# Optimization experiments

Hardware: AMD Instinct MI355X
Metric: run time of the kernel (lower is better)

Reference implementation:

```python
import jax, jax.numpy as jnp
import numpy as np

H = 1024          # hidden_size
NH = 16           # num_attention_heads
HD = H // NH      # attention_head_size (= rotary_dim)
I = 4096          # intermediate_size
E = 8             # num_experts
TOPK = 2          # top_k_experts
EPS = 1e-12       # layer_norm_eps
B, S = 2, 2048


def setup_inputs() -> dict:
    key = jax.random.key(0)
    ks = jax.random.split(key, 12)
    sc = 0.02
    return {
        "hidden_states": jax.random.normal(ks[0], (B, S, H), dtype=jnp.float32),
        "Wq": jax.random.normal(ks[1], (H, H), dtype=jnp.float32) * sc,
        "Wk": jax.random.normal(ks[2], (H, H), dtype=jnp.float32) * sc,
        "Wv": jax.random.normal(ks[3], (H, H), dtype=jnp.float32) * sc,
        "Wd": jax.random.normal(ks[4], (H, H), dtype=jnp.float32) * sc,
        "bd": jnp.zeros((H,), dtype=jnp.float32),
        "ln1_g": jnp.ones((H,), dtype=jnp.float32),
        "ln1_b": jnp.zeros((H,), dtype=jnp.float32),
        "Wg": jax.random.normal(ks[5], (H, E), dtype=jnp.float32) * sc,
        "W1": jax.random.normal(ks[6], (E, H, I), dtype=jnp.float32) * sc,
        "W2": jax.random.normal(ks[7], (E, I, H), dtype=jnp.float32) * sc,
        "ln2_g": jnp.ones((H,), dtype=jnp.float32),
        "ln2_b": jnp.zeros((H,), dtype=jnp.float32),
    }


def _layernorm(x, g, b):
    mu = jnp.mean(x, axis=-1, keepdims=True)
    var = jnp.mean(jnp.square(x - mu), axis=-1, keepdims=True)
    return (x - mu) * jax.lax.rsqrt(var + EPS) * g + b


def _rotate_half(x):
    x1, x2 = x[..., : HD // 2], x[..., HD // 2 :]
    return jnp.concatenate((-x2, x1), axis=-1)


def _rope_cos_sin(seq_len, dtype):
    inv_freq = 1.0 / (10000.0 ** (jnp.arange(0, HD, 2, dtype=jnp.float32) / HD))
    t = jnp.arange(seq_len, dtype=jnp.float32)
    freqs = jnp.einsum("i,j->ij", t, inv_freq)          # [S, HD/2]
    emb = jnp.concatenate((freqs, freqs), axis=-1)        # [S, HD]
    return jnp.cos(emb).astype(dtype)[None, None], jnp.sin(emb).astype(dtype)[None, None]


def reference(hidden_states, Wq, Wk, Wv, Wd, bd, ln1_g, ln1_b, Wg, W1, W2, ln2_g, ln2_b):
    b, s, h = hidden_states.shape
    x = hidden_states

    # ---- multi-head attention with RoPE ----
    def heads(z):  # [B,S,H] -> [B,NH,S,HD]
        return z.reshape(b, s, NH, HD).transpose(0, 2, 1, 3)

    q = heads(x @ Wq)
    k = heads(x @ Wk)
    v = heads(x @ Wv)
    cos, sin = _rope_cos_sin(s, q.dtype)
    q = q * cos + _rotate_half(q) * sin
    k = k * cos + _rotate_half(k) * sin

    scores = jnp.einsum("bnqd,bnkd->bnqk", q, k) / jnp.sqrt(jnp.float32(HD)).astype(q.dtype)
    probs = jax.nn.softmax(scores, axis=-1)
    ctx = jnp.einsum("bnqk,bnkd->bnqd", probs, v)
    ctx = ctx.transpose(0, 2, 1, 3).reshape(b, s, h)

    attn_out = ctx @ Wd + bd
    hs = _layernorm(attn_out + x, ln1_g, ln1_b)  # residual + LN

    # ---- MoE ----
    T = b * s
    xt = hs.reshape(T, h)
    router_logits = xt @ Wg                                   # [T, E]
    probs_r = jax.nn.softmax(router_logits.astype(jnp.float32), axis=-1)
    rw, sel = jax.lax.top_k(probs_r, TOPK)                    # [T, K]
    rw = rw / jnp.sum(rw, axis=-1, keepdims=True)

    # aux load-balancing loss
    f_i = jnp.sum(jax.nn.one_hot(sel, E, dtype=jnp.float32), axis=(0, 1)) / T
    P_i = jnp.mean(probs_r, axis=0)
    aux_loss = E * jnp.sum(f_i * P_i)

    # per-token combine weights [T, E] (0 for unrouted experts)
    combine = jnp.zeros((T, E), dtype=jnp.float32)
    combine = combine.at[jnp.arange(T)[:, None], sel].add(rw)
    combine = combine.astype(xt.dtype)

    moe_out = jnp.zeros_like(xt)
    for e in range(E):  # small fixed expert loop
        ye = jax.nn.gelu(xt @ W1[e], approximate=False) @ W2[e]
        moe_out = moe_out + combine[:, e : e + 1] * ye
    moe_out = moe_out.reshape(b, s, h)

    out = _layernorm(hs + moe_out, ln2_g, ln2_b)
    return out, aux_loss
```

## Files before the change

### kernel.cpp

```cpp
#include <hip/hip_runtime.h>
#include <hip/hip_bf16.h>
#include <math.h>

#define H_ 1024
#define NH_ 16
#define HD_ 64
#define I_ 4096
#define E_ 8
#define B_ 2
#define S_ 2048
#define T_ 4096

#define MAXSLOTS 9216
#define MAXTILES 72

typedef __attribute__((ext_vector_type(8))) short short8v;
typedef __attribute__((ext_vector_type(4))) float f32x4;

#define GLOAD16(g, l) __builtin_amdgcn_global_load_lds((const __attribute__((address_space(1))) void*)(g), (__attribute__((address_space(3))) void*)(l), 16, 0, 0)

static __device__ inline unsigned short f2bf(float x) {
    __hip_bfloat16 h = __float2bfloat16(x);
    unsigned short u;
    __builtin_memcpy(&u, &h, 2);
    return u;
}
static __device__ inline float bf2f(unsigned short u) {
    __hip_bfloat16 h;
    __builtin_memcpy(&h, &u, 2);
    return __bfloat162float(h);
}

static __device__ inline float gelu_fast(float x) {
    float z  = x * 0.70710678118654752f;
    float az = fabsf(z);
    float t  = __builtin_amdgcn_rcpf(fmaf(0.3275911f, az, 1.f));
    float p  = fmaf(1.061405429f, t, -1.453152027f);
    p = fmaf(p, t, 1.421413741f);
    p = fmaf(p, t, -0.284496736f);
    p = fmaf(p, t, 0.254829592f);
    p = p * t;
    float e = __expf(-az*az);
    float er = 1.f - p*e;
    er = (z < 0.f) ? -er : er;
    return 0.5f * x * (1.f + er);
}

__global__ void zero_kernel(float* __restrict__ p, int n) {
    int i = blockIdx.x * blockDim.x + threadIdx.x;
    if (i < n) p[i] = 0.f;
}

__global__ __launch_bounds__(256) void split_bf16(
    const float* __restrict__ in, __hip_bfloat16* __restrict__ hi,
    __hip_bfloat16* __restrict__ lo, int n4)
{
    int i = blockIdx.x * blockDim.x + threadIdx.x;
    if (i >= n4) return;
    float4 v = ((const float4*)in)[i];
    unsigned short h0 = f2bf(v.x), h1 = f2bf(v.y), h2 = f2bf(v.z), h3 = f2bf(v.w);
    unsigned short l0 = f2bf(v.x - bf2f(h0)), l1 = f2bf(v.y - bf2f(h1));
    unsigned short l2 = f2bf(v.z - bf2f(h2)), l3 = f2bf(v.w - bf2f(h3));
    uint2 ph = make_uint2((unsigned)h0 | ((unsigned)h1 << 16), (unsigned)h2 | ((unsigned)h3 << 16));
    uint2 pl = make_uint2((unsigned)l0 | ((unsigned)l1 << 16), (unsigned)l2 | ((unsigned)l3 << 16));
    *(uint2*)((char*)hi + (size_t)i*8) = ph;
    *(uint2*)((char*)lo + (size_t)i*8) = pl;
}

__global__ __launch_bounds__(256) void transpose_split_w4(
    const float* __restrict__ Wq, const float* __restrict__ Wk,
    const float* __restrict__ Wv, const float* __restrict__ Wd,
    __hip_bfloat16* __restrict__ wqkv_h, __hip_bfloat16* __restrict__ wqkv_l,
    __hip_bfloat16* __restrict__ wd_h, __hip_bfloat16* __restrict__ wd_l)
{
    __shared__ float t[64][65];
    const int z = blockIdx.z;
    const float* in = (z==0) ? Wq : (z==1) ? Wk : (z==2) ? Wv : Wd;
    __hip_bfloat16* oh = (z<3) ? (wqkv_h + (size_t)z*1024*1024) : wd_h;
    __hip_bfloat16* ol = (z<3) ? (wqkv_l + (size_t)z*1024*1024) : wd_l;
    int k0 = blockIdx.y*64, n0 = blockIdx.x*64;
    int tid = threadIdx.x;
    #pragma unroll
    for (int it=0; it<4; ++it) {
        int lin = it*256 + tid;
        int r = lin >> 4, c4 = (lin & 15) << 2;
        float4 v = *(const float4*)&in[(size_t)(k0+r)*1024 + n0 + c4];
        t[r][c4] = v.x; t[r][c4+1] = v.y; t[r][c4+2] = v.z; t[r][c4+3] = v.w;
    }
    __syncthreads();
    #pragma unroll
    for (int it=0; it<4; ++it) {
        int lin = it*256 + tid;
        int r = lin >> 4, c4 = (lin & 15) << 2;
        float v0 = t[c4][r], v1 = t[c4+1][r], v2 = t[c4+2][r], v3 = t[c4+3][r];
        ushort4 hh, ll;
        hh.x = f2bf(v0); hh.y = f2bf(v1); hh.z = f2bf(v2); hh.w = f2bf(v3);
        ll.x = f2bf(v0 - bf2f(hh.x)); ll.y = f2bf(v1 - bf2f(hh.y));
        ll.z = f2bf(v2 - bf2f(hh.z)); ll.w = f2bf(v3 - bf2f(hh.w));
        size_t o = (size_t)(n0+r)*1024 + k0 + c4;
        *(ushort4*)&oh[o] = hh;
        *(ushort4*)&ol[o] = ll;
    }
}

__global__ __launch_bounds__(256) void transpose_bf16(
    const float* __restrict__ in, __hip_bfloat16* __restrict__ outp, int K, int N)
{
    __shared__ float t[64][65];
    size_t eoff = (size_t)blockIdx.z * (size_t)K * (size_t)N;
    int k0 = blockIdx.y*64, n0 = blockIdx.x*64;
    int tid = threadIdx.x;
    #pragma unroll
    for (int it=0; it<4; ++it) {
        int lin = it*256 + tid;
        int r = lin >> 4, c4 = (lin & 15) << 2;
        float4 v = *(const float4*)&in[eoff + (size_t)(k0+r)*N + n0 + c4];
        t[r][c4] = v.x; t[r][c4+1] = v.y; t[r][c4+2] = v.z; t[r][c4+3] = v.w;
    }
    __syncthreads();
    #pragma unroll
    for (int it=0; it<4; ++it) {
        int lin = it*256 + tid;
        int r = lin >> 4, c4 = (lin & 15) << 2;
        ushort4 o;
        o.x = f2bf(t[c4][r]);   o.y = f2bf(t[c4+1][r]);
        o.z = f2bf(t[c4+2][r]); o.w = f2bf(t[c4+3][r]);
        *(ushort4*)&outp[eoff + (size_t)(n0+r)*K + k0 + c4] = o;
    }
}

template<bool BIAS>
__global__ __launch_bounds__(256, 2) void gemm_bf16x3(
    const __hip_bfloat16* __restrict__ Ah, const __hip_bfloat16* __restrict__ Al,
    const __hip_bfloat16* __restrict__ Bh, const __hip_bfloat16* __restrict__ Bl,
    float* __restrict__ C, const float* __restrict__ bias, int N, int K, int nbx)
{
    const int tid = threadIdx.x;
    const int w = tid >> 6, lane = tid & 63;
    const int wg = blockIdx.x;
    const int xcd = wg & 7, ix = wg >> 3;
    const int byc = (int)(gridDim.x >> 3) / nbx;
    const int by = xcd*byc + ix / nbx;
    const int bx = ix % nbx;

    __shared__ __align__(16) char smem[65536];
    const int AH = 0, AL = 16384, BH = 32768, BL = 49152;

    const int laneg = lane >> 3;
    const int k2sw = ((lane & 7) ^ laneg) << 4;
    const int l15 = lane & 15, l4 = lane >> 4;
    const int wr = w >> 1, wc = w & 1;

    f32x4 acc[4][4];
    #pragma unroll
    for (int m=0;m<4;m++)
        #pragma unroll
        for (int n=0;n<4;n++) acc[m][n] = (f32x4){0.f,0.f,0.f,0.f};

    for (int k0 = 0; k0 < K; k0 += 64) {
        __syncthreads();
        #pragma unroll
        for (int qq=0;qq<4;qq++) {
            int arow = by*128 + (w*4+qq)*8 + laneg;
            int brow = bx*128 + (w*4+qq)*8 + laneg;
            size_t aoff = ((size_t)arow*K + k0)*2 + k2sw;
            size_t boff = ((size_t)brow*K + k0)*2 + k2sw;
            GLOAD16((const char*)Ah + aoff, smem + AH + (w*4+qq)*1024);
            GLOAD16((const char*)Al + aoff, smem + AL + (w*4+qq)*1024);
            GLOAD16((const char*)Bh + boff, smem + BH + (w*4+qq)*1024);
            GLOAD16((const char*)Bl + boff, smem + BL + (w*4+qq)*1024);
        }
        __syncthreads();

        short8v ahf[4][2], alf[4][2], bhf[4][2], blf[4][2];
        #pragma unroll
        for (int m=0;m<4;m++) {
            int row = wr*64 + m*16 + l15;
            int rb = row << 7, rsw = (row & 7) << 4;
            #pragma unroll
            for (int s=0;s<2;s++) {
                int off = rb + ((s*64 + (l4<<4)) ^ rsw);
                ahf[m][s] = *(const short8v*)(smem + AH + off);
                alf[m][s] = *(const short8v*)(smem + AL + off);
            }
        }
        #pragma unroll
        for (int n=0;n<4;n++) {
            int row = wc*64 + n*16 + l15;
            int rb = row << 7, rsw = (row & 7) << 4;
            #pragma unroll
            for (int s=0;s<2;s++) {
                int off = rb + ((s*64 + (l4<<4)) ^ rsw);
                bhf[n][s] = *(const short8v*)(smem + BH + off);
                blf[n][s] = *(const short8v*)(smem + BL + off);
            }
        }
        #pragma unroll
        for (int m=0;m<4;m++)
            #pragma unroll
            for (int n=0;n<4;n++)
                #pragma unroll
                for (int s=0;s<2;s++) {
                    acc[m][n] = __builtin_amdgcn_mfma_f32_16x16x32_bf16(ahf[m][s], bhf[n][s], acc[m][n], 0, 0, 0);
                    acc[m][n] = __builtin_amdgcn_mfma_f32_16x16x32_bf16(ahf[m][s], blf[n][s], acc[m][n], 0, 0, 0);
                    acc[m][n] = __builtin_amdgcn_mfma_f32_16x16x32_bf16(alf[m][s], bhf[n][s], acc[m][n], 0, 0, 0);
                }
    }

    #pragma unroll
    for (int m=0;m<4;m++)
        #pragma unroll
        for (int j=0;j<4;j++) {
            int orow = by*128 + wr*64 + m*16 + l4*4 + j;
            #pragma unroll
            for (int n=0;n<4;n++) {
                int ocol = bx*128 + wc*64 + n*16 + l15;
                float v = acc[m][n][j];
                if (BIAS) v += bias[ocol];
                C[(size_t)orow*N + ocol] = v;
            }
        }
}

template<int MODE, bool PE>
__global__ __launch_bounds__(256) void moe_mfma(
    const __hip_bfloat16* __restrict__ A,
    const __hip_bfloat16* __restrict__ Bt,
    __hip_bfloat16* __restrict__ y1,
    float* __restrict__ moe_out,
    const int* __restrict__ slot_token,
    const float* __restrict__ slot_w,
    const int* __restrict__ tile_expert,
    const int* __restrict__ cnt_ptr,
    const int* __restrict__ base_ptr,
    int N, int K, int nbx)
{
    const int tid = threadIdx.x;
    const int w = tid >> 6, lane = tid & 63;

    int bx, slot0, y1row0;
    const __hip_bfloat16* Bp;
    if (PE) {
        bx = blockIdx.x;
        int tloc = blockIdx.y;
        if ((tloc << 7) >= *cnt_ptr) return;
        slot0 = *base_ptr + (tloc << 7);
        y1row0 = tloc << 7;
        Bp = Bt;
    } else {
        const int wg = blockIdx.x;
        const int xcd = wg & 7, ix = wg >> 3;
        const int byc = (int)(gridDim.x >> 3) / nbx;
        int gt = xcd*byc + ix % byc;
        bx = ix / byc;
        if (gt >= *cnt_ptr) return;
        int e = tile_expert[gt];
        Bp = Bt + (size_t)e * (size_t)K * (size_t)N;
        slot0 = gt << 7;
        y1row0 = gt << 7;
    }

    __shared__ __align__(16) char smem[32768];

    const int laneg = lane >> 3;
    const int k2sw = ((lane & 7) ^ laneg) << 4;

    int tokq[4];
    if (MODE == 2) {
        #pragma unroll
        for (int qq=0;qq<4;qq++) {
            int t0 = slot_token[slot0 + (w*4+qq)*8 + laneg];
            tokq[qq] = t0 < 0 ? 0 : t0;
        }
    }

    f32x4 acc[4][4];
    #pragma unroll
    for (int m=0;m<4;m++)
        #pragma unroll
        for (int n=0;n<4;n++) acc[m][n] = (f32x4){0.f,0.f,0.f,0.f};

    const int l15 = lane & 15;
    const int l4  = lane >> 4;
    const int wr = w >> 1, wc = w & 1;

    for (int k0 = 0; k0 < K; k0 += 64) {
        __syncthreads();
        #pragma unroll
        for (int qq=0;qq<4;qq++) {
            const char* ga;
            if (MODE == 2) {
                ga = (const char*)A + (((size_t)tokq[qq])*K + k0)*2 + k2sw;
            } else {
                int row = y1row0 + (w*4+qq)*8 + laneg;
                ga = (const char*)A + ((size_t)row*K + k0)*2 + k2sw;
            }
            GLOAD16(ga, smem + (w*4+qq)*1024);
        }
        #pragma unroll
        for (int qq=0;qq<4;qq++) {
            int row = bx*128 + (w*4+qq)*8 + laneg;
            const char* gb = (const char*)Bp + ((size_t)row*K + k0)*2 + k2sw;
            GLOAD16(gb, smem + 16384 + (w*4+qq)*1024);
        }
        __syncthreads();

        short8v a_frag[4][2], b_frag[4][2];
        #pragma unroll
        for (int m=0;m<4;m++) {
            int row = wr*64 + m*16 + l15;
            int rb = row << 7;
            #pragma unroll
            for (int s=0;s<2;s++) {
                int off = rb + ((s*64 + (l4<<4)) ^ ((row&7)<<4));
                a_frag[m][s] = *(const short8v*)(smem + off);
            }
        }
        #pragma unroll
        for (int n=0;n<4;n++) {
            int row = wc*64 + n*16 + l15;
            int rb = row << 7;
            #pragma unroll
            for (int s=0;s<2;s++) {
                int off = rb + ((s*64 + (l4<<4)) ^ ((row&7)<<4));
                b_frag[n][s] = *(const short8v*)(smem + 16384 + off);
            }
        }
        #pragma unroll
        for (int m=0;m<4;m++)
            #pragma unroll
            for (int n=0;n<4;n++) {
                acc[m][n] = __builtin_amdgcn_mfma_f32_16x16x32_bf16(a_frag[m][0], b_frag[n][0], acc[m][n], 0, 0, 0);
                acc[m][n] = __builtin_amdgcn_mfma_f32_16x16x32_bf16(a_frag[m][1], b_frag[n][1], acc[m][n], 0, 0, 0);
            }
    }

    if (MODE == 3) {
        #pragma unroll
        for (int m=0;m<4;m++) {
            #pragma unroll
            for (int j=0;j<4;j++) {
                int orow = wr*64 + m*16 + l4*4 + j;
                int slot = slot0 + orow;
                int tok = slot_token[slot];
                if (tok < 0) continue;
                float sw = slot_w[slot];
                #pragma unroll
                for (int n=0;n<4;n++) {
                    int ocol = bx*128 + wc*64 + n*16 + l15;
                    atomicAdd(&moe_out[(size_t)tok*H_ + ocol], sw * acc[m][n][j]);
                }
            }
        }
    } else {
        __syncthreads();
        #pragma unroll
        for (int m=0;m<4;m++)
            #pragma unroll
            for (int j=0;j<4;j++) {
                int orow = wr*64 + m*16 + l4*4 + j;
                #pragma unroll
                for (int n=0;n<4;n++) {
                    int ocol = wc*64 + n*16 + l15;
                    unsigned short g = f2bf(gelu_fast(acc[m][n][j]));
                    *(unsigned short*)(smem + orow*256 + ocol*2) = g;
                }
            }
        __syncthreads();
        #pragma unroll
        for (int s=0;s<8;s++) {
            int row = w*32 + s*4 + l4;
            short8v v = *(const short8v*)(smem + row*256 + l15*16);
            *(short8v*)((char*)y1 + ((size_t)(y1row0 + row)*N + bx*128 + l15*8)*2) = v;
        }
    }
}

__global__ void rope_split_kernel(
    const float* __restrict__ qkv,
    __hip_bfloat16* __restrict__ qh, __hip_bfloat16* __restrict__ ql,
    __hip_bfloat16* __restrict__ kh, __hip_bfloat16* __restrict__ kl)
{
    int idx = blockIdx.x * blockDim.x + threadIdx.x;
    int i = idx & 31;
    int n = (idx >> 5) & (NH_-1);
    int t = idx >> 9;
    int b = t >> 11;
    int pos = t & (S_ - 1);
    float inv = exp2f((float)i * (-13.287712379549449f / 32.f));
    float ang = (float)pos * inv;
    float c = cosf(ang), s = sinf(ang);
    size_t base = (size_t)t*3072 + (size_t)n*64;
    size_t obase = ((size_t)(b*NH_ + n)*S_ + pos)*64;

    float q1 = qkv[base+i], q2 = qkv[base+i+32];
    float qo1 = (q1*c - q2*s)*0.125f;
    float qo2 = (q2*c + q1*s)*0.125f;
    unsigned short h1 = f2bf(qo1), h2 = f2bf(qo2);
    qh[obase+i]    = *(__hip_bfloat16*)&h1;
    qh[obase+i+32] = *(__hip_bfloat16*)&h2;
    unsigned short lo1 = f2bf(qo1 - bf2f(h1)), lo2 = f2bf(qo2 - bf2f(h2));
    ql[obase+i]    = *(__hip_bfloat16*)&lo1;
    ql[obase+i+32] = *(__hip_bfloat16*)&lo2;

    float k1 = qkv[base+1024+i], k2 = qkv[base+1024+i+32];
    float ko1 = k1*c - k2*s;
    float ko2 = k2*c + k1*s;
    unsigned short kh1 = f2bf(ko1), kh2 = f2bf(ko2);
    kh[obase+i]    = *(__hip_bfloat16*)&kh1;
    kh[obase+i+32] = *(__hip_bfloat16*)&kh2;
    unsigned short kl1 = f2bf(ko1 - bf2f(kh1)), kl2 = f2bf(ko2 - bf2f(kh2));
    kl[obase+i]    = *(__hip_bfloat16*)&kl1;
    kl[obase+i+32] = *(__hip_bfloat16*)&kl2;
}

__global__ __launch_bounds__(256) void vsplit_t_kernel(
    const float* __restrict__ qkv,
    __hip_bfloat16* __restrict__ vth, __hip_bfloat16* __restrict__ vtl)
{
    __shared__ float t[64][65];
    const int s0 = blockIdx.x*64;
    const int hn = blockIdx.y;
    const int b  = blockIdx.z;
    const int tid = threadIdx.x;
    #pragma unroll
    for (int it=0; it<4; ++it) {
        int lin = it*256 + tid;
        int r = lin >> 4, c4 = (lin & 15) << 2;
        float4 vv = *(const float4*)&qkv[(size_t)(b*S_ + s0 + r)*3072 + 2048 + hn*64 + c4];
        t[r][c4] = vv.x; t[r][c4+1] = vv.y; t[r][c4+2] = vv.z; t[r][c4+3] = vv.w;
    }
    __syncthreads();
    size_t obase = (size_t)(b*NH_ + hn)*64*S_;
    #pragma unroll
    for (int it=0; it<4; ++it) {
        int lin = it*256 + tid;
        int d = lin >> 4, c4 = (lin & 15) << 2;
        float v0 = t[c4][d], v1 = t[c4+1][d], v2 = t[c4+2][d], v3 = t[c4+3][d];
        ushort4 hh, ll;
        hh.x = f2bf(v0); hh.y = f2bf(v1); hh.z = f2bf(v2); hh.w = f2bf(v3);
        ll.x = f2bf(v0 - bf2f(hh.x)); ll.y = f2bf(v1 - bf2f(hh.y));
        ll.z = f2bf(v2 - bf2f(hh.z)); ll.w = f2bf(v3 - bf2f(hh.w));
        size_t o = obase + (size_t)d*S_ + s0 + c4;
        *(ushort4*)&vth[o] = hh;
        *(ushort4*)&vtl[o] = ll;
    }
}

__global__ __launch_bounds__(256) void attn_mfma(
    const __hip_bfloat16* __restrict__ qh, const __hip_bfloat16* __restrict__ ql,
    const __hip_bfloat16* __restrict__ kh, const __hip_bfloat16* __restrict__ kl,
    const __hip_bfloat16* __restrict__ vth, const __hip_bfloat16* __restrict__ vtl,
    __hip_bfloat16* __restrict__ ctx_hi, __hip_bfloat16* __restrict__ ctx_lo)
{
    const int wg = blockIdx.x;
    const int xcd = wg & 7;
    const int ix = wg >> 3;
    const int head = xcd*4 + (ix >> 5);
    const int qt = ix & 31;
    const int b = head >> 4, hn = head & 15;

    const int tid = threadIdx.x;
    const int w = tid >> 6, lane = tid & 63;
    const int l15 = lane & 15, l4 = lane >> 4;
    const int laneg = lane >> 3;
    const int k2sw = ((lane & 7) ^ laneg) << 4;

    __shared__ __align__(16) char smem[32768];
    const int KHo = 0, KLo = 8192, VHo = 16384, VLo = 24576;
    const int PHo = 0, PLo = 8192;

    const size_t kbase = (size_t)head*S_*64;
    const size_t vbase = (size_t)head*64*S_;

    #pragma unroll
    for (int qq=0;qq<2;qq++) {
        int c = w*2 + qq;
        int row = qt*64 + c*8 + laneg;
        size_t off = (kbase + (size_t)row*64)*2 + k2sw;
        GLOAD16((const char*)qh + off, smem + KHo + c*1024);
        GLOAD16((const char*)ql + off, smem + KLo + c*1024);
    }
    __syncthreads();
    short8v qhf[2], qlf[2];
    {
        int row = w*16 + l15;
        int rsw = (row & 7) << 4;
        #pragma unroll
        for (int s=0;s<2;s++) {
            int off = row*128 + ((s*64 + l4*16) ^ rsw);
            qhf[s] = *(const short8v*)(smem + KHo + off);
            qlf[s] = *(const short8v*)(smem + KLo + off);
        }
    }

    f32x4 acc[4];
    #pragma unroll
    for (int db=0;db<4;db++) acc[db] = (f32x4){0.f,0.f,0.f,0.f};
    float lrun[4] = {0.f, 0.f, 0.f, 0.f};

    for (int kt=0; kt<S_/64; ++kt) {
        __syncthreads();
        #pragma unroll
        for (int qq=0;qq<2;qq++) {
            int c = w*2 + qq;
            int r8 = c*8 + laneg;
            size_t koff = (kbase + (size_t)(kt*64 + r8)*64)*2 + k2sw;
            GLOAD16((const char*)kh + koff, smem + KHo + c*1024);
            GLOAD16((const char*)kl + koff, smem + KLo + c*1024);
            size_t voff = (vbase + (size_t)r8*S_ + kt*64)*2 + k2sw;
            GLOAD16((const char*)vth + voff, smem + VHo + c*1024);
            GLOAD16((const char*)vtl + voff, smem + VLo + c*1024);
        }
        __syncthreads();

        f32x4 s_acc[4];
        #pragma unroll
        for (int cb=0;cb<4;cb++) {
            s_acc[cb] = (f32x4){0.f,0.f,0.f,0.f};
            int row = cb*16 + l15;
            int rsw = (row & 7) << 4;
            #pragma unroll
            for (int s=0;s<2;s++) {
                int off = row*128 + ((s*64 + l4*16) ^ rsw);
                short8v khf = *(const short8v*)(smem + KHo + off);
                short8v klf = *(const short8v*)(smem + KLo + off);
                s_acc[cb] = __builtin_amdgcn_mfma_f32_16x16x32_bf16(qhf[s], khf, s_acc[cb], 0, 0, 0);
                s_acc[cb] = __builtin_amdgcn_mfma_f32_16x16x32_bf16(qhf[s], klf, s_acc[cb], 0, 0, 0);
                s_acc[cb] = __builtin_amdgcn_mfma_f32_16x16x32_bf16(qlf[s], khf, s_acc[cb], 0, 0, 0);
            }
        }
        __syncthreads();

        #pragma unroll
        for (int cb=0;cb<4;cb++)
            #pragma unroll
            for (int j=0;j<4;j++) {
                float p = __expf(s_acc[cb][j]);
                lrun[j] += p;
                int prow = w*16 + l4*4 + j;
                unsigned short hh = f2bf(p);
                unsigned short ll = f2bf(p - bf2f(hh));
                int off = prow*128 + (((cb*16 + l15)*2) ^ ((prow&7)<<4));
                *(unsigned short*)(smem + PHo + off) = hh;
                *(unsigned short*)(smem + PLo + off) = ll;
            }
        asm volatile("s_waitcnt lgkmcnt(0)" ::: "memory");
        __builtin_amdgcn_sched_barrier(0);

        short8v pah[2], pal[2];
        {
            int row = w*16 + l15;
            int rsw = (row & 7) << 4;
            #pragma unroll
            for (int s=0;s<2;s++) {
                int off = row*128 + ((s*64 + l4*16) ^ rsw);
                pah[s] = *(const short8v*)(smem + PHo + off);
                pal[s] = *(const short8v*)(smem + PLo + off);
            }
        }
        #pragma unroll
        for (int db=0;db<4;db++) {
            int row = db*16 + l15;
            int rsw = (row & 7) << 4;
            #pragma unroll
            for (int s=0;s<2;s++) {
                int off = row*128 + ((s*64 + l4*16) ^ rsw);
                short8v vhf = *(const short8v*)(smem + VHo + off);
                short8v vlf = *(const short8v*)(smem + VLo + off);
                acc[db] = __builtin_amdgcn_mfma_f32_16x16x32_bf16(pah[s], vhf, acc[db], 0, 0, 0);
                acc[db] = __builtin_amdgcn_mfma_f32_16x16x32_bf16(pah[s], vlf, acc[db], 0, 0, 0);
                acc[db] = __builtin_amdgcn_mfma_f32_16x16x32_bf16(pal[s], vhf, acc[db], 0, 0, 0);
            }
        }
    }

    #pragma unroll
    for (int j=0;j<4;j++) {
        float s = lrun[j];
        #pragma unroll
        for (int m=8;m;m>>=1) s += __shfl_xor(s, m);
        lrun[j] = s;
    }

    #pragma unroll
    for (int db=0;db<4;db++)
        #pragma unroll
        for (int j=0;j<4;j++) {
            int qrow = qt*64 + w*16 + l4*4 + j;
            float o = acc[db][j] / lrun[j];
            unsigned short hh = f2bf(o);
            unsigned short ll = f2bf(o - bf2f(hh));
            size_t oidx = (size_t)(b*S_ + qrow)*H_ + hn*64 + db*16 + l15;
            ctx_hi[oidx] = *(__hip_bfloat16*)&hh;
            ctx_lo[oidx] = *(__hip_bfloat16*)&ll;
        }
}

__global__ __launch_bounds__(256) void ln_kernel(
    const float* __restrict__ a, const float* __restrict__ res,
    const float* __restrict__ g, const float* __restrict__ beta,
    float* __restrict__ out, __hip_bfloat16* __restrict__ outb)
{
    int row = blockIdx.x, tid = threadIdx.x;
    const float4 va = ((const float4*)(a + (size_t)row*H_))[tid];
    const float4 vr = ((const float4*)(res + (size_t)row*H_))[tid];
    float x0=va.x+vr.x, x1=va.y+vr.y, x2=va.z+vr.z, x3=va.w+vr.w;
    float s  = x0+x1+x2+x3;
    float ss = x0*x0 + x1*x1 + x2*x2 + x3*x3;
    #pragma unroll
    for (int off=32; off; off>>=1) { s += __shfl_xor(s, off); ss += __shfl_xor(ss, off); }
    __shared__ float red[8];
    if ((tid&63)==0) { red[tid>>6]=s; red[4+(tid>>6)]=ss; }
    __syncthreads();
    if (tid==0) { red[0]=red[0]+red[1]+red[2]+red[3]; red[4]=red[4]+red[5]+red[6]+red[7]; }
    __syncthreads();
    float mu  = red[0] * (1.f/H_);
    float var = red[4] * (1.f/H_) - mu*mu;
    float rs = rsqrtf(fmaxf(var, 0.f) + 1e-12f);
    const float4 vg = ((const float4*)g)[tid];
    const float4 vb = ((const float4*)beta)[tid];
    float4 vo;
    vo.x = (x0-mu)*rs*vg.x + vb.x;
    vo.y = (x1-mu)*rs*vg.y + vb.y;
    vo.z = (x2-mu)*rs*vg.z + vb.z;
    vo.w = (x3-mu)*rs*vg.w + vb.w;
    ((float4*)(out + (size_t)row*H_))[tid] = vo;
    if (outb) {
        unsigned int p0 = (unsigned)f2bf(vo.x) | ((unsigned)f2bf(vo.y) << 16);
        unsigned int p1 = (unsigned)f2bf(vo.z) | ((unsigned)f2bf(vo.w) << 16);
        ((uint2*)(outb + (size_t)row*H_))[tid] = make_uint2(p0, p1);
    }
}

__global__ __launch_bounds__(256) void router_kernel(
    const float* __restrict__ hs, const float* __restrict__ Wg,
    int* __restrict__ tok_e, float* __restrict__ tok_w,
    int* __restrict__ counts, float* __restrict__ P_sum)
{
    const int w = threadIdx.x >> 6, lane = threadIdx.x & 63;
    float psum[E_];
    int cnt[E_];
    #pragma unroll
    for (int e=0;e<E_;e++){ psum[e]=0.f; cnt[e]=0; }

    for (int it=0; it<16; ++it) {
        int t = blockIdx.x*64 + it*4 + w;
        const float* row = hs + (size_t)t * H_;
        float acc[E_];
        #pragma unroll
        for (int e=0;e<E_;e++) acc[e]=0.f;
        for (int i16=0; i16<16; ++i16) {
            int i = i16*64 + lane;
            float xv = row[i];
            const float* wg = Wg + (size_t)i*E_;
            #pragma unroll
            for (int e=0;e<E_;e++) acc[e] = fmaf(xv, wg[e], acc[e]);
        }
        #pragma unroll
        for (int e=0;e<E_;e++) {
            float vv = acc[e];
            #pragma unroll
            for (int off=32; off; off>>=1) vv += __shfl_xor(vv, off);
            acc[e] = vv;
        }
        float mx = acc[0];
        #pragma unroll
        for (int e=1;e<E_;e++) mx = fmaxf(mx, acc[e]);
        float p[E_], se=0.f;
        #pragma unroll
        for (int e=0;e<E_;e++){ p[e] = __expf(acc[e]-mx); se += p[e]; }
        float isv = 1.f/se;
        #pragma unroll
        for (int e=0;e<E_;e++){ p[e]*=isv; psum[e] += p[e]; }
        int e1=0;
        #pragma unroll
        for (int e=1;e<E_;e++) if (p[e] > p[e1]) e1=e;
        int e2 = (e1==0)?1:0;
        #pragma unroll
        for (int e=0;e<E_;e++) if (e!=e1 && p[e] > p[e2]) e2=e;
        #pragma unroll
        for (int e=0;e<E_;e++) cnt[e] += (e==e1?1:0) + (e==e2?1:0);
        if (lane==0) {
            float w1=p[e1], w2=p[e2], si=1.f/(w1+w2);
            tok_e[t*2]=e1; tok_e[t*2+1]=e2;
            tok_w[t*2]=w1*si; tok_w[t*2+1]=w2*si;
        }
    }
    if (lane==0) {
        #pragma unroll
        for (int e=0;e<E_;e++) {
            atomicAdd(&P_sum[e], psum[e]);
            atomicAdd(&counts[e], cnt[e]);
        }
    }
}

__global__ void router_finalize(
    const int* __restrict__ counts, const float* __restrict__ P_sum,
    int* __restrict__ base, int* __restrict__ cursor,
    int* __restrict__ cnt_pad, int* __restrict__ ntiles,
    int* __restrict__ slot_token, int* __restrict__ tile_expert,
    float* __restrict__ aux_out)
{
    __shared__ int sbase[E_+1];
    if (threadIdx.x == 0) {
        int bacc = 0;
        float aux = 0.f;
        for (int e=0;e<E_;e++) {
            sbase[e] = bacc; base[e] = bacc;
            int cp = (counts[e] + 127) & ~127;
            cnt_pad[e] = cp;
            bacc += cp;
            cursor[e] = 0;
            aux += ((float)counts[e]/(float)T_) * (P_sum[e]/(float)T_);
        }
        sbase[E_] = bacc;
        *ntiles = bacc >> 7;
        *aux_out = (float)E_ * aux;
    }
    __syncthreads();
    for (int sIdx = (int)threadIdx.x; sIdx < MAXSLOTS; sIdx += (int)blockDim.x)
        slot_token[sIdx] = -1;
    for (int tt = (int)threadIdx.x; tt < MAXTILES; tt += (int)blockDim.x) {
        int s = tt*128;
        int e = E_-1;
        for (int qe=0; qe<E_; ++qe) if (s < sbase[qe+1]) { e = qe; break; }
        tile_expert[tt] = e;
    }
}

__global__ void scatter_slots(
    const int* __restrict__ tok_e, const float* __restrict__ tok_w,
    const int* __restrict__ base, int* __restrict__ cursor,
    int* __restrict__ slot_token, float* __restrict__ slot_w)
{
    int t = blockIdx.x*blockDim.x + threadIdx.x;
    if (t >= T_) return;
    #pragma unroll
    for (int j=0;j<2;j++) {
        int e = tok_e[t*2+j];
        int pos = atomicAdd(&cursor[e], 1);
        int s = base[e] + pos;
        slot_token[s] = t;
        slot_w[s] = tok_w[t*2+j];
    }
}

extern "C" void kernel_launch(void* const* d_in, const int* in_sizes, int n_in,
                              void* d_out, int out_size, void* d_ws, size_t ws_size,
                              hipStream_t stream)
{
    const float* x    = (const float*)d_in[0];
    const float* Wq   = (const float*)d_in[1];
    const float* Wk   = (const float*)d_in[2];
    const float* Wv   = (const float*)d_in[3];
    const float* Wd   = (const float*)d_in[4];
    const float* bd   = (const float*)d_in[5];
    const float* ln1g = (const float*)d_in[6];
    const float* ln1b = (const float*)d_in[7];
    const float* Wg   = (const float*)d_in[8];
    const float* W1   = (const float*)d_in[9];
    const float* W2   = (const float*)d_in[10];
    const float* ln2g = (const float*)d_in[11];
    const float* ln2b = (const float*)d_in[12];
    float* out = (float*)d_out;

    float* f0 = (float*)d_ws;
    const size_t M1 = 1u << 20;
    float* qkv      = f0;
    float* attn_out = f0 + 12*M1;
    float* hs       = f0;
    float* moe_out  = f0 + 4*M1;
    __hip_bfloat16* hs_b = (__hip_bfloat16*)(f0 + 16*M1);

    float* misc = f0 + 18*M1;
    int*   misc_i = (int*)misc;
    int*   tok_e   = misc_i;
    float* tok_w   = misc + 8192;
    int*   slot_tok= misc_i + 16384;
    float* slot_w  = misc + 25600;
    int*   counts  = misc_i + 34816;
    float* P_sum   = misc + 34824;
    int*   cursor  = misc_i + 34832;
    int*   basep   = misc_i + 34840;
    int*   cnt_pad = misc_i + 34848;
    int*   ntiles  = misc_i + 34856;
    int*   tile_ex = misc_i + 34857;

    float* off_p = f0 + 18*M1 + 65536;
    __hip_bfloat16* xa_hi = (__hip_bfloat16*)(off_p);
    __hip_bfloat16* xa_lo = (__hip_bfloat16*)(off_p + 2*M1);
    __hip_bfloat16* at_qh = (__hip_bfloat16*)(off_p + 4*M1);
    __hip_bfloat16* at_ql = (__hip_bfloat16*)(off_p + 6*M1);
    __hip_bfloat16* at_kh = (__hip_bfloat16*)(off_p + 8*M1);
    __hip_bfloat16* at_kl = (__hip_bfloat16*)(off_p + 10*M1);
    __hip_bfloat16* at_vh = (__hip_bfloat16*)(off_p + 12*M1);
    __hip_bfloat16* at_vl = (__hip_bfloat16*)(off_p + 14*M1);
    __hip_bfloat16* wqkv_h = (__hip_bfloat16*)(off_p + 16*M1);
    __hip_bfloat16* wqkv_l = (__hip_bfloat16*)(off_p + 16*M1 + 3*(M1/2));
    __hip_bfloat16* wd_h = (__hip_bfloat16*)(off_p + 19*M1);
    __hip_bfloat16* wd_l = (__hip_bfloat16*)(off_p + 19*M1 + M1/2);

    float* wreg = off_p + 4*M1;
    const bool FULL = ws_size >= (size_t)300*1024*1024;

    dim3 blk(256);

    split_bf16<<<(T_*H_/4)/256, blk, 0, stream>>>(x, xa_hi, xa_lo, T_*H_/4);
    transpose_split_w4<<<dim3(16,16,4), blk, 0, stream>>>(Wq, Wk, Wv, Wd, wqkv_h, wqkv_l, wd_h, wd_l);

    gemm_bf16x3<false><<<dim3(768), blk, 0, stream>>>(xa_hi, xa_lo, wqkv_h, wqkv_l, qkv, nullptr, 3072, H_, 24);

    rope_split_kernel<<<(T_*NH_*32)/256, blk, 0, stream>>>(qkv, at_qh, at_ql, at_kh, at_kl);
    vsplit_t_kernel<<<dim3(S_/64, NH_, B_), blk, 0, stream>>>(qkv, at_vh, at_vl);

    attn_mfma<<<dim3(B_*NH_*(S_/64)), blk, 0, stream>>>(at_qh, at_ql, at_kh, at_kl, at_vh, at_vl, xa_hi, xa_lo);

    gemm_bf16x3<true><<<dim3(256), blk, 0, stream>>>(xa_hi, xa_lo, wd_h, wd_l, attn_out, bd, H_, H_, 8);

    zero_kernel<<<(T_*H_)/256, blk, 0, stream>>>(moe_out, T_*H_);
    zero_kernel<<<1, blk, 0, stream>>>(misc + 34816, 16);

    ln_kernel<<<T_, blk, 0, stream>>>(attn_out, x, ln1g, ln1b, hs, hs_b);

    router_kernel<<<T_/64, blk, 0, stream>>>(hs, Wg, tok_e, tok_w, counts, P_sum);
    router_finalize<<<1, blk, 0, stream>>>(counts, P_sum, basep, cursor, cnt_pad, ntiles,
                                           slot_tok, tile_ex, out + (size_t)T_*H_);
    scatter_slots<<<T_/256, blk, 0, stream>>>(tok_e, tok_w, basep, cursor, slot_tok, slot_w);

    if (FULL) {
        __hip_bfloat16* W1t = (__hip_bfloat16*)wreg;
        __hip_bfloat16* W2t = (__hip_bfloat16*)(wreg + 16*M1);
        __hip_bfloat16* y1  = (__hip_bfloat16*)(wreg + 32*M1);
        transpose_bf16<<<dim3(I_/64, H_/64, E_), blk, 0, stream>>>(W1, W1t, H_, I_);
        transpose_bf16<<<dim3(H_/64, I_/64, E_), blk, 0, stream>>>(W2, W2t, I_, H_);
        moe_mfma<2,false><<<dim3(MAXTILES*32), blk, 0, stream>>>(
            hs_b, W1t, y1, nullptr, slot_tok, slot_w, tile_ex, ntiles, nullptr, I_, H_, 32);
        moe_mfma<3,false><<<dim3(MAXTILES*8), blk, 0, stream>>>(
            y1, W2t, nullptr, moe_out, slot_tok, slot_w, tile_ex, ntiles, nullptr, H_, I_, 8);
    } else {
        __hip_bfloat16* w1t = (__hip_bfloat16*)wreg;
        __hip_bfloat16* w2t = (__hip_bfloat16*)(wreg + 2*M1);
        __hip_bfloat16* y1  = (__hip_bfloat16*)(wreg + 4*M1);
        for (int e=0; e<E_; ++e) {
            transpose_bf16<<<dim3(I_/64, H_/64, 1), blk, 0, stream>>>(W1 + (size_t)e*H_*I_, w1t, H_, I_);
            moe_mfma<2,true><<<dim3(I_/128, 32), blk, 0, stream>>>(
                hs_b, w1t, y1, nullptr, slot_tok, slot_w, nullptr, cnt_pad+e, basep+e, I_, H_, 0);
            transpose_bf16<<<dim3(H_/64, I_/64, 1), blk, 0, stream>>>(W2 + (size_t)e*I_*H_, w2t, I_, H_);
            moe_mfma<3,true><<<dim3(H_/128, 32), blk, 0, stream>>>(
                y1, w2t, nullptr, moe_out, slot_tok, slot_w, nullptr, cnt_pad+e, basep+e, H_, I_, 0);
        }
    }

    ln_kernel<<<T_, blk, 0, stream>>>(moe_out, hs, ln2g, ln2b, out, nullptr);
}
```

Measured before the change: 762.6 us.

## Fuse prep kernels and overlap MoE weight transposes with the QKV GEMM

Merges the input split and the QKV/Wd weight transpose-split into one launch, merges RoPE with the V transpose-split, and merges the two zeroing kernels. In the full-workspace path, the W1/W2 expert transposes move into the same grid as the QKV GEMM as extra blocks, so the memory-bound transposes can fill the GPU alongside the compute-bound GEMM. Workspace buffers are relaid so y1 and the transposed weights do not overlap buffers still in use. The fused GEMM kernel uses launch_bounds of 2, which may change register allocation compared with the standalone GEMM.

```diff
diff --git a/kernel.cpp b/kernel.cpp
--- a/kernel.cpp
+++ b/kernel.cpp
@@ -46,40 +46,41 @@
     return 0.5f * x * (1.f + er);
 }
 
-__global__ void zero_kernel(float* __restrict__ p, int n) {
+__global__ void zero_all(float* __restrict__ p, int n, float* __restrict__ misc16) {
     int i = blockIdx.x * blockDim.x + threadIdx.x;
     if (i < n) p[i] = 0.f;
-}
-
-__global__ __launch_bounds__(256) void split_bf16(
-    const float* __restrict__ in, __hip_bfloat16* __restrict__ hi,
-    __hip_bfloat16* __restrict__ lo, int n4)
-{
-    int i = blockIdx.x * blockDim.x + threadIdx.x;
-    if (i >= n4) return;
-    float4 v = ((const float4*)in)[i];
-    unsigned short h0 = f2bf(v.x), h1 = f2bf(v.y), h2 = f2bf(v.z), h3 = f2bf(v.w);
-    unsigned short l0 = f2bf(v.x - bf2f(h0)), l1 = f2bf(v.y - bf2f(h1));
-    unsigned short l2 = f2bf(v.z - bf2f(h2)), l3 = f2bf(v.w - bf2f(h3));
-    uint2 ph = make_uint2((unsigned)h0 | ((unsigned)h1 << 16), (unsigned)h2 | ((unsigned)h3 << 16));
-    uint2 pl = make_uint2((unsigned)l0 | ((unsigned)l1 << 16), (unsigned)l2 | ((unsigned)l3 << 16));
-    *(uint2*)((char*)hi + (size_t)i*8) = ph;
-    *(uint2*)((char*)lo + (size_t)i*8) = pl;
-}
-
-__global__ __launch_bounds__(256) void transpose_split_w4(
+    if (blockIdx.x == 0 && threadIdx.x < 16) misc16[threadIdx.x] = 0.f;
+}
+
+__global__ __launch_bounds__(256) void prep_inputs(
+    const float* __restrict__ x,
     const float* __restrict__ Wq, const float* __restrict__ Wk,
     const float* __restrict__ Wv, const float* __restrict__ Wd,
+    __hip_bfloat16* __restrict__ xa_hi, __hip_bfloat16* __restrict__ xa_lo,
     __hip_bfloat16* __restrict__ wqkv_h, __hip_bfloat16* __restrict__ wqkv_l,
     __hip_bfloat16* __restrict__ wd_h, __hip_bfloat16* __restrict__ wd_l)
 {
     __shared__ float t[64][65];
-    const int z = blockIdx.z;
+    const int bid = blockIdx.x;
+    const int tid = threadIdx.x;
+    if (bid < 4096) {
+        int i = bid * 256 + tid;
+        float4 v = ((const float4*)x)[i];
+        unsigned short h0 = f2bf(v.x), h1 = f2bf(v.y), h2 = f2bf(v.z), h3 = f2bf(v.w);
+        unsigned short l0 = f2bf(v.x - bf2f(h0)), l1 = f2bf(v.y - bf2f(h1));
+        unsigned short l2 = f2bf(v.z - bf2f(h2)), l3 = f2bf(v.w - bf2f(h3));
+        uint2 ph = make_uint2((unsigned)h0 | ((unsigned)h1 << 16), (unsigned)h2 | ((unsigned)h3 << 16));
+        uint2 pl = make_uint2((unsigned)l0 | ((unsigned)l1 << 16), (unsigned)l2 | ((unsigned)l3 << 16));
+        *(uint2*)((char*)xa_hi + (size_t)i*8) = ph;
+        *(uint2*)((char*)xa_lo + (size_t)i*8) = pl;
+        return;
+    }
+    int tt = bid - 4096;
+    int bx = tt & 15, by = (tt >> 4) & 15, z = tt >> 8;
     const float* in = (z==0) ? Wq : (z==1) ? Wk : (z==2) ? Wv : Wd;
     __hip_bfloat16* oh = (z<3) ? (wqkv_h + (size_t)z*1024*1024) : wd_h;
     __hip_bfloat16* ol = (z<3) ? (wqkv_l + (size_t)z*1024*1024) : wd_l;
-    int k0 = blockIdx.y*64, n0 = blockIdx.x*64;
-    int tid = threadIdx.x;
+    int k0 = by*64, n0 = bx*64;
     #pragma unroll
     for (int it=0; it<4; ++it) {
         int lin = it*256 + tid;
@@ -220,6 +221,132 @@
                 C[(size_t)orow*N + ocol] = v;
             }
         }
+}
+
+__global__ __launch_bounds__(256, 2) void fused_qkv_w12(
+    const __hip_bfloat16* __restrict__ Ah, const __hip_bfloat16* __restrict__ Al,
+    const __hip_bfloat16* __restrict__ Bh, const __hip_bfloat16* __restrict__ Bl,
+    float* __restrict__ C,
+    const float* __restrict__ W1, const float* __restrict__ W2,
+    __hip_bfloat16* __restrict__ W1t, __hip_bfloat16* __restrict__ W2t)
+{
+    __shared__ __align__(16) char smem[65536];
+    const int tid = threadIdx.x;
+    const int bid = blockIdx.x;
+
+    if (bid < 768) {
+        const int N = 3072, K = 1024;
+        const int w = tid >> 6, lane = tid & 63;
+        const int xcd = bid & 7, ix = bid >> 3;
+        const int by = xcd*4 + ix / 24;
+        const int bx = ix % 24;
+        const int AH = 0, AL = 16384, BH = 32768, BL = 49152;
+        const int laneg = lane >> 3;
+        const int k2sw = ((lane & 7) ^ laneg) << 4;
+        const int l15 = lane & 15, l4 = lane >> 4;
+        const int wr = w >> 1, wc = w & 1;
+
+        f32x4 acc[4][4];
+        #pragma unroll
+        for (int m=0;m<4;m++)
+            #pragma unroll
+            for (int n=0;n<4;n++) acc[m][n] = (f32x4){0.f,0.f,0.f,0.f};
+
+        for (int k0 = 0; k0 < K; k0 += 64) {
+            __syncthreads();
+            #pragma unroll
+            for (int qq=0;qq<4;qq++) {
+                int arow = by*128 + (w*4+qq)*8 + laneg;
+                int brow = bx*128 + (w*4+qq)*8 + laneg;
+                size_t aoff = ((size_t)arow*K + k0)*2 + k2sw;
+                size_t boff = ((size_t)brow*K + k0)*2 + k2sw;
+                GLOAD16((const char*)Ah + aoff, smem + AH + (w*4+qq)*1024);
+                GLOAD16((const char*)Al + aoff, smem + AL + (w*4+qq)*1024);
+                GLOAD16((const char*)Bh + boff, smem + BH + (w*4+qq)*1024);
+                GLOAD16((const char*)Bl + boff, smem + BL + (w*4+qq)*1024);
+            }
+            __syncthreads();
+
+            short8v ahf[4][2], alf[4][2], bhf[4][2], blf[4][2];
+            #pragma unroll
+            for (int m=0;m<4;m++) {
+                int row = wr*64 + m*16 + l15;
+                int rb = row << 7, rsw = (row & 7) << 4;
+                #pragma unroll
+                for (int s=0;s<2;s++) {
+                    int off = rb + ((s*64 + (l4<<4)) ^ rsw);
+                    ahf[m][s] = *(const short8v*)(smem + AH + off);
+                    alf[m][s] = *(const short8v*)(smem + AL + off);
+                }
+            }
+            #pragma unroll
+            for (int n=0;n<4;n++) {
+                int row = wc*64 + n*16 + l15;
+                int rb = row << 7, rsw = (row & 7) << 4;
+                #pragma unroll
+                for (int s=0;s<2;s++) {
+                    int off = rb + ((s*64 + (l4<<4)) ^ rsw);
+                    bhf[n][s] = *(const short8v*)(smem + BH + off);
+                    blf[n][s] = *(const short8v*)(smem + BL + off);
+                }
+            }
+            #pragma unroll
+            for (int m=0;m<4;m++)
+                #pragma unroll
+                for (int n=0;n<4;n++)
+                    #pragma unroll
+                    for (int s=0;s<2;s++) {
+                        acc[m][n] = __builtin_amdgcn_mfma_f32_16x16x32_bf16(ahf[m][s], bhf[n][s], acc[m][n], 0, 0, 0);
+                        acc[m][n] = __builtin_amdgcn_mfma_f32_16x16x32_bf16(ahf[m][s], blf[n][s], acc[m][n], 0, 0, 0);
+                        acc[m][n] = __builtin_amdgcn_mfma_f32_16x16x32_bf16(alf[m][s], bhf[n][s], acc[m][n], 0, 0, 0);
+                    }
+        }
+
+        #pragma unroll
+        for (int m=0;m<4;m++)
+            #pragma unroll
+            for (int j=0;j<4;j++) {
+                int orow = by*128 + wr*64 + m*16 + l4*4 + j;
+                #pragma unroll
+                for (int n=0;n<4;n++) {
+                    int ocol = bx*128 + wc*64 + n*16 + l15;
+                    C[(size_t)orow*N + ocol] = acc[m][n][j];
+                }
+            }
+        return;
+    }
+
+    int t = bid - 768;
+    const float* src;
+    __hip_bfloat16* dst;
+    int K, N;
+    if (t < 8192) { src = W1; dst = W1t; K = 1024; N = 4096; }
+    else          { t -= 8192; src = W2; dst = W2t; K = 4096; N = 1024; }
+    const int nb_n = N >> 6;
+    int bx = t % nb_n;
+    int rest = t / nb_n;
+    int by = rest % (K >> 6);
+    int bz = rest / (K >> 6);
+    size_t eoff = (size_t)bz * (size_t)K * (size_t)N;
+    int k0 = by*64, n0 = bx*64;
+    float (*tt)[65] = (float(*)[65])smem;
+    #pragma unroll
+    for (int it=0; it<4; ++it) {
+        int lin = it*256 + tid;
+        int r = lin >> 4, c4 = (lin & 15) << 2;
+        float4 v = *(const float4*)&src[eoff + (size_t)(k0+r)*N + n0 + c4];
+        tt[r][c4] = v.x; tt[r][c4+1] = v.y; tt[r][c4+2] = v.z; tt[r][c4+3] = v.w;
+    }
+    __syncthreads();
+    #pragma unroll
+    for (int it=0; it<4; ++it) {
+        int lin = it*256 + tid;
+        int r = lin >> 4, c4 = (lin & 15) << 2;
+        ushort4 o;
+        o.x = f2bf(tt[c4][r]);   o.y = f2bf(tt[c4+1][r]);
+        o.z = f2bf(tt[c4+2][r]); o.w = f2bf(tt[c4+3][r]);
+        *(ushort4*)&dst[eoff + (size_t)(n0+r)*K + k0 + c4] = o;
+    }
 }
 
 template<int MODE, bool PE>
@@ -376,53 +503,53 @@
     }
 }
 
-__global__ void rope_split_kernel(
+__global__ __launch_bounds__(256) void rope_vsplit(
     const float* __restrict__ qkv,
     __hip_bfloat16* __restrict__ qh, __hip_bfloat16* __restrict__ ql,
-    __hip_bfloat16* __restrict__ kh, __hip_bfloat16* __restrict__ kl)
-{
-    int idx = blockIdx.x * blockDim.x + threadIdx.x;
-    int i = idx & 31;
-    int n = (idx >> 5) & (NH_-1);
-    int t = idx >> 9;
-    int b = t >> 11;
-    int pos = t & (S_ - 1);
-    float inv = exp2f((float)i * (-13.287712379549449f / 32.f));
-    float ang = (float)pos * inv;
-    float c = cosf(ang), s = sinf(ang);
-    size_t base = (size_t)t*3072 + (size_t)n*64;
-    size_t obase = ((size_t)(b*NH_ + n)*S_ + pos)*64;
-
-    float q1 = qkv[base+i], q2 = qkv[base+i+32];
-    float qo1 = (q1*c - q2*s)*0.125f;
-    float qo2 = (q2*c + q1*s)*0.125f;
-    unsigned short h1 = f2bf(qo1), h2 = f2bf(qo2);
-    qh[obase+i]    = *(__hip_bfloat16*)&h1;
-    qh[obase+i+32] = *(__hip_bfloat16*)&h2;
-    unsigned short lo1 = f2bf(qo1 - bf2f(h1)), lo2 = f2bf(qo2 - bf2f(h2));
-    ql[obase+i]    = *(__hip_bfloat16*)&lo1;
-    ql[obase+i+32] = *(__hip_bfloat16*)&lo2;
-
-    float k1 = qkv[base+1024+i], k2 = qkv[base+1024+i+32];
-    float ko1 = k1*c - k2*s;
-    float ko2 = k2*c + k1*s;
-    unsigned short kh1 = f2bf(ko1), kh2 = f2bf(ko2);
-    kh[obase+i]    = *(__hip_bfloat16*)&kh1;
-    kh[obase+i+32] = *(__hip_bfloat16*)&kh2;
-    unsigned short kl1 = f2bf(ko1 - bf2f(kh1)), kl2 = f2bf(ko2 - bf2f(kh2));
-    kl[obase+i]    = *(__hip_bfloat16*)&kl1;
-    kl[obase+i+32] = *(__hip_bfloat16*)&kl2;
-}
-
-__global__ __launch_bounds__(256) void vsplit_t_kernel(
-    const float* __restrict__ qkv,
+    __hip_bfloat16* __restrict__ kh, __hip_bfloat16* __restrict__ kl,
     __hip_bfloat16* __restrict__ vth, __hip_bfloat16* __restrict__ vtl)
 {
     __shared__ float t[64][65];
-    const int s0 = blockIdx.x*64;
-    const int hn = blockIdx.y;
-    const int b  = blockIdx.z;
+    const int bid = blockIdx.x;
     const int tid = threadIdx.x;
+    if (bid < 8192) {
+        int idx = bid * 256 + tid;
+        int i = idx & 31;
+        int n = (idx >> 5) & (NH_-1);
+        int tk = idx >> 9;
+        int b = tk >> 11;
+        int pos = tk & (S_ - 1);
+        float inv = exp2f((float)i * (-13.287712379549449f / 32.f));
+        float ang = (float)pos * inv;
+        float c = cosf(ang), s = sinf(ang);
+        size_t base = (size_t)tk*3072 + (size_t)n*64;
+        size_t obase = ((size_t)(b*NH_ + n)*S_ + pos)*64;
+
+        float q1 = qkv[base+i], q2 = qkv[base+i+32];
+        float qo1 = (q1*c - q2*s)*0.125f;
+        float qo2 = (q2*c + q1*s)*0.125f;
+        unsigned short h1 = f2bf(qo1), h2 = f2bf(qo2);
+        qh[obase+i]    = *(__hip_bfloat16*)&h1;
+        qh[obase+i+32] = *(__hip_bfloat16*)&h2;
+        unsigned short lo1 = f2bf(qo1 - bf2f(h1)), lo2 = f2bf(qo2 - bf2f(h2));
+        ql[obase+i]    = *(__hip_bfloat16*)&lo1;
+        ql[obase+i+32] = *(__hip_bfloat16*)&lo2;
+
+        float k1 = qkv[base+1024+i], k2 = qkv[base+1024+i+32];
+        float ko1 = k1*c - k2*s;
+        float ko2 = k2*c + k1*s;
+        unsigned short kh1 = f2bf(ko1), kh2 = f2bf(ko2);
+        kh[obase+i]    = *(__hip_bfloat16*)&kh1;
+        kh[obase+i+32] = *(__hip_bfloat16*)&kh2;
+        unsigned short kl1 = f2bf(ko1 - bf2f(kh1)), kl2 = f2bf(ko2 - bf2f(kh2));
+        kl[obase+i]    = *(__hip_bfloat16*)&kl1;
+        kl[obase+i+32] = *(__hip_bfloat16*)&kl2;
+        return;
+    }
+    int tt = bid - 8192;
+    const int s0 = (tt & 31)*64;
+    const int hn = (tt >> 5) & 15;
+    const int b  = tt >> 9;
     #pragma unroll
     for (int it=0; it<4; ++it) {
         int lin = it*256 + tid;
@@ -802,25 +929,30 @@
     __hip_bfloat16* wd_h = (__hip_bfloat16*)(off_p + 19*M1);
     __hip_bfloat16* wd_l = (__hip_bfloat16*)(off_p + 19*M1 + M1/2);
 
+    const bool FULL = ws_size >= (size_t)300*1024*1024;
+    __hip_bfloat16* W1t = (__hip_bfloat16*)(off_p + 20*M1);
+    __hip_bfloat16* W2t = (__hip_bfloat16*)(off_p + 36*M1);
+    __hip_bfloat16* y1F = (__hip_bfloat16*)(off_p);
     float* wreg = off_p + 4*M1;
-    const bool FULL = ws_size >= (size_t)300*1024*1024;
 
     dim3 blk(256);
 
-    split_bf16<<<(T_*H_/4)/256, blk, 0, stream>>>(x, xa_hi, xa_lo, T_*H_/4);
-    transpose_split_w4<<<dim3(16,16,4), blk, 0, stream>>>(Wq, Wk, Wv, Wd, wqkv_h, wqkv_l, wd_h, wd_l);
-
-    gemm_bf16x3<false><<<dim3(768), blk, 0, stream>>>(xa_hi, xa_lo, wqkv_h, wqkv_l, qkv, nullptr, 3072, H_, 24);
-
-    rope_split_kernel<<<(T_*NH_*32)/256, blk, 0, stream>>>(qkv, at_qh, at_ql, at_kh, at_kl);
-    vsplit_t_kernel<<<dim3(S_/64, NH_, B_), blk, 0, stream>>>(qkv, at_vh, at_vl);
+    prep_inputs<<<dim3(5120), blk, 0, stream>>>(x, Wq, Wk, Wv, Wd, xa_hi, xa_lo, wqkv_h, wqkv_l, wd_h, wd_l);
+
+    if (FULL) {
+        fused_qkv_w12<<<dim3(768 + 8192 + 8192), blk, 0, stream>>>(
+            xa_hi, xa_lo, wqkv_h, wqkv_l, qkv, W1, W2, W1t, W2t);
+    } else {
+        gemm_bf16x3<false><<<dim3(768), blk, 0, stream>>>(xa_hi, xa_lo, wqkv_h, wqkv_l, qkv, nullptr, 3072, H_, 24);
+    }
+
+    rope_vsplit<<<dim3(8192 + 1024), blk, 0, stream>>>(qkv, at_qh, at_ql, at_kh, at_kl, at_vh, at_vl);
 
     attn_mfma<<<dim3(B_*NH_*(S_/64)), blk, 0, stream>>>(at_qh, at_ql, at_kh, at_kl, at_vh, at_vl, xa_hi, xa_lo);
 
     gemm_bf16x3<true><<<dim3(256), blk, 0, stream>>>(xa_hi, xa_lo, wd_h, wd_l, attn_out, bd, H_, H_, 8);
 
-    zero_kernel<<<(T_*H_)/256, blk, 0, stream>>>(moe_out, T_*H_);
-    zero_kernel<<<1, blk, 0, stream>>>(misc + 34816, 16);
+    zero_all<<<dim3((T_*H_)/256), blk, 0, stream>>>(moe_out, T_*H_, misc + 34816);
 
     ln_kernel<<<T_, blk, 0, stream>>>(attn_out, x, ln1g, ln1b, hs, hs_b);
 
@@ -830,15 +962,10 @@
     scatter_slots<<<T_/256, blk, 0, stream>>>(tok_e, tok_w, basep, cursor, slot_tok, slot_w);
 
     if (FULL) {
-        __hip_bfloat16* W1t = (__hip_bfloat16*)wreg;
-        __hip_bfloat16* W2t = (__hip_bfloat16*)(wreg + 16*M1);
-        __hip_bfloat16* y1  = (__hip_bfloat16*)(wreg + 32*M1);
-        transpose_bf16<<<dim3(I_/64, H_/64, E_), blk, 0, stream>>>(W1, W1t, H_, I_);
-        transpose_bf16<<<dim3(H_/64, I_/64, E_), blk, 0, stream>>>(W2, W2t, I_, H_);
         moe_mfma<2,false><<<dim3(MAXTILES*32), blk, 0, stream>>>(
-            hs_b, W1t, y1, nullptr, slot_tok, slot_w, tile_ex, ntiles, nullptr, I_, H_, 32);
+            hs_b, W1t, y1F, nullptr, slot_tok, slot_w, tile_ex, ntiles, nullptr, I_, H_, 32);
         moe_mfma<3,false><<<dim3(MAXTILES*8), blk, 0, stream>>>(
-            y1, W2t, nullptr, moe_out, slot_tok, slot_w, tile_ex, ntiles, nullptr, H_, I_, 8);
+            y1F, W2t, nullptr, moe_out, slot_tok, slot_w, tile_ex, ntiles, nullptr, H_, I_, 8);
     } else {
         __hip_bfloat16* w1t = (__hip_bfloat16*)wreg;
         __hip_bfloat16* w2t = (__hip_bfloat16*)(wreg + 2*M1);
```

New measurement: 756.5 us. No clear change (-0.8%).
